# Kernel optimization log

Measured on AMD Instinct MI355X. Metric: run time of the kernel, lower is better.

Reference implementation:

```python
import jax, jax.numpy as jnp
import numpy as np

B, C, H, W = 4, 256, 160, 160
N = 512
REID = 128
NUM_LAYERS = 2
BINS = 7          # adaptive_avg_pool2d target (7,7)
EPS_BN = 1e-5
EPS_NORM = 1e-12  # torch F.normalize eps


def setup_inputs() -> dict:
    key = jax.random.key(0)
    ks = jax.random.split(key, 8)
    x = jax.random.normal(ks[0], (B, C, H, W), jnp.float32)
    # valid normalized boxes: x1,y1 in [0,0.7], w,h in [0.1,0.3]
    xy1 = jax.random.uniform(ks[1], (B, N, 2), minval=0.0, maxval=0.7)
    wh = jax.random.uniform(ks[2], (B, N, 2), minval=0.1, maxval=0.3)
    bboxes = jnp.concatenate([xy1, jnp.minimum(xy1 + wh, 1.0)], axis=-1)
    # conv stack params (kaiming-ish init), BN in eval mode with running stats
    conv_w = jax.random.normal(ks[3], (NUM_LAYERS, C, C, 3, 3), jnp.float32) * np.sqrt(2.0 / (C * 9)).astype(np.float32)
    conv_b = jnp.zeros((NUM_LAYERS, C), jnp.float32)
    bn_gamma = jnp.ones((NUM_LAYERS, C), jnp.float32)
    bn_beta = jnp.zeros((NUM_LAYERS, C), jnp.float32)
    bn_mean = jnp.zeros((NUM_LAYERS, C), jnp.float32)
    bn_var = jnp.ones((NUM_LAYERS, C), jnp.float32)
    # reid_embedding MLP: Linear(C, C//2) -> ReLU -> Dropout(eval) -> Linear(C//2, REID)
    w1 = jax.random.normal(ks[4], (C // 2, C), jnp.float32) * 0.01
    b1 = jnp.zeros((C // 2,), jnp.float32)
    w2 = jax.random.normal(ks[5], (REID, C // 2), jnp.float32) * 0.01
    b2 = jnp.zeros((REID,), jnp.float32)
    return dict(x=x, bboxes=bboxes, conv_w=conv_w, conv_b=conv_b,
                bn_gamma=bn_gamma, bn_beta=bn_beta, bn_mean=bn_mean, bn_var=bn_var,
                w1=w1, b1=b1, w2=w2, b2=b2)


def _conv_bn_relu(x, w, b, gamma, beta, mean, var):
    y = jax.lax.conv_general_dilated(
        x, w, window_strides=(1, 1), padding=((1, 1), (1, 1)),
        dimension_numbers=('NCHW', 'OIHW', 'NCHW')) + b[None, :, None, None]
    scale = (gamma / jnp.sqrt(var + EPS_BN))[None, :, None, None]
    y = (y - mean[None, :, None, None]) * scale + beta[None, :, None, None]
    return jax.nn.relu(y)


def _roi_pool(S, box):
    # S: (C, H+1, W+1) integral image of the feature map; box: (4,) = x1,y1,x2,y2 in [0,1]
    x1 = jnp.clip(jnp.floor(box[0] * W).astype(jnp.int32), 0, W)
    y1 = jnp.clip(jnp.floor(box[1] * H).astype(jnp.int32), 0, H)
    x2 = jnp.clip(jnp.floor(box[2] * W).astype(jnp.int32), 0, W)
    y2 = jnp.clip(jnp.floor(box[3] * H).astype(jnp.int32), 0, H)
    valid = (x2 > x1) & (y2 > y1)
    hl = jnp.maximum(y2 - y1, 1)
    wl = jnp.maximum(x2 - x1, 1)
    i = jnp.arange(BINS)
    # PyTorch adaptive_avg_pool2d binning: [floor(i*L/B), ceil((i+1)*L/B))
    hs = y1 + (i * hl) // BINS
    he = y1 + ((i + 1) * hl + BINS - 1) // BINS
    ws = x1 + (i * wl) // BINS
    we = x1 + ((i + 1) * wl + BINS - 1) // BINS
    # bin sums via integral image -> (C, 7, 7)
    s = (S[:, he[:, None], we[None, :]] - S[:, hs[:, None], we[None, :]]
         - S[:, he[:, None], ws[None, :]] + S[:, hs[:, None], ws[None, :]])
    area = ((he - hs)[:, None] * (we - ws)[None, :]).astype(S.dtype)
    # adaptive 7x7 avg pool, then global avg pool over the 7x7 grid
    pooled = jnp.mean(s / area, axis=(1, 2))  # (C,)
    return pooled, valid


def reference(x, bboxes, conv_w, conv_b, bn_gamma, bn_beta, bn_mean, bn_var, w1, b1, w2, b2):
    f = x
    for l in range(NUM_LAYERS):
        f = _conv_bn_relu(f, conv_w[l], conv_b[l], bn_gamma[l], bn_beta[l], bn_mean[l], bn_var[l])
    # integral image, zero-padded: S[b,c,y,x] = sum of f[b,c,:y,:x] -> (B, C, H+1, W+1)
    S = jnp.pad(jnp.cumsum(jnp.cumsum(f, axis=2), axis=3), ((0, 0), (0, 0), (1, 0), (1, 0)))
    pooled, valid = jax.vmap(jax.vmap(_roi_pool, in_axes=(None, 0)), in_axes=(0, 0))(S, bboxes)
    # reid_embedding MLP (dropout is identity in eval)
    h = jax.nn.relu(jnp.einsum('bnc,hc->bnh', pooled, w1) + b1)
    feat = jnp.einsum('bnh,rh->bnr', h, w2) + b2
    feat = jnp.where(valid[..., None], feat, jnp.zeros((), feat.dtype))
    norm = jnp.maximum(jnp.linalg.norm(feat, axis=-1, keepdims=True), EPS_NORM)
    return feat / norm
```

## Files before the change

kernel.cpp:

```cpp
#include <hip/hip_runtime.h>
#include <hip/hip_bf16.h>

typedef __attribute__((ext_vector_type(8))) short s16x8;
typedef __attribute__((ext_vector_type(4))) float f32x4;


__device__ __forceinline__ void async_ld16(const void* g, void* l) {
  __builtin_amdgcn_global_load_lds(
      (const __attribute__((address_space(1))) void*)g,
      (__attribute__((address_space(3))) void*)l, 16, 0, 0);
}

__global__ __launch_bounds__(256) void zero_borders(__hip_bfloat16* __restrict__ xpad,
                                                    __hip_bfloat16* __restrict__ f1) {
  int bi = blockIdx.x;
  int buf = bi / 2576; int rem = bi - buf * 2576;
  int b = rem / 644;   int e = rem - b * 644;
  int y, x;
  if (e < 162)      { y = 0;           x = e; }
  else if (e < 324) { y = 161;         x = e - 162; }
  else if (e < 484) { y = e - 324 + 1; x = 0; }
  else              { y = e - 484 + 1; x = 161; }
  __hip_bfloat16* p = (buf ? f1 : xpad) + (((size_t)b * 162 + y) * 162 + x) * 256 + threadIdx.x;
  *p = __float2bfloat16(0.f);
}

__global__ __launch_bounds__(256) void nchw2nhwc(const float* __restrict__ x,
                                                 __hip_bfloat16* __restrict__ xpad) {
  __shared__ float tile[32][33];
  int blk = blockIdx.x;
  int xt = blk % 5;
  int ct = (blk / 5) & 7;
  int by = blk / 40;
  int b = by / 160, y = by - (by / 160) * 160;
  int tx = threadIdx.x, ty = threadIdx.y;
  const float* src = x + (((size_t)(b * 256 + ct * 32)) * 160 + y) * 160 + xt * 32 + tx;
#pragma unroll
  for (int k = 0; k < 4; k++) tile[ty * 4 + k][tx] = src[(size_t)(ty * 4 + k) * 25600];
  __syncthreads();
  __hip_bfloat16* dst = xpad + (((size_t)(b * 162 + y + 1)) * 162 + (xt * 32 + 1)) * 256 + ct * 32 + tx;
#pragma unroll
  for (int k = 0; k < 4; k++) {
    int xx = ty * 4 + k;
    dst[(size_t)xx * 256] = __float2bfloat16(tile[tx][xx]);
  }
}

__global__ __launch_bounds__(256) void pack_w(const float* __restrict__ cw,
                                              __hip_bfloat16* __restrict__ wpk) {
  int t = blockIdx.x * 256 + threadIdx.x;
  int ci = t & 255, co = (t >> 8) & 255, rest = t >> 16;
  int tap = rest % 9, l = rest / 9;
  int dy = tap / 3, dx = tap - dy * 3;
  float v = cw[((((size_t)l * 256 + co) * 256 + ci) * 3 + dy) * 3 + dx];
  wpk[(((size_t)l * 9 + tap) * 256 + co) * 256 + ci] = __float2bfloat16(v);
}

__global__ void prep_bn(const float* __restrict__ cb, const float* __restrict__ g,
                        const float* __restrict__ bt, const float* __restrict__ mn,
                        const float* __restrict__ vr, float* __restrict__ ab) {
  int t = blockIdx.x * 256 + threadIdx.x;
  float a = g[t] / sqrtf(vr[t] + 1e-5f);
  ab[t] = a;
  ab[512 + t] = (cb[t] - mn[t]) * a + bt[t];
}

__global__ __launch_bounds__(256) void pack_mlp(const float* __restrict__ w1,
                                                const float* __restrict__ w2,
                                                float* __restrict__ w1t,
                                                float* __restrict__ w2t) {
  int t = blockIdx.x * 256 + threadIdx.x;
  if (t < 32768) {
    int h = t >> 8, k = t & 255;
    w1t[k * 128 + h] = w1[h * 256 + k];
  } else {
    int u = t - 32768;
    int r = u >> 7, k = u & 127;
    w2t[k * 128 + r] = w2[r * 128 + k];
  }
}

__global__ __launch_bounds__(256, 2) void conv_bn_relu(
    const __hip_bfloat16* __restrict__ inp, __hip_bfloat16* __restrict__ outp,
    const __hip_bfloat16* __restrict__ wpk,
    const float* __restrict__ alpha, const float* __restrict__ beff) {
  __shared__ __align__(16) short As[128 * 64];
  __shared__ __align__(16) short Bs[256 * 64];
  const int t = threadIdx.x;
  const int mtile = ((blockIdx.x & 7) * 100) + (blockIdx.x >> 3);
  const int l = t & 63;
  const int wv = t >> 6;
  const int lr = l & 15, lq = l >> 4;
  const int wm = wv >> 1, wn = wv & 1;

  const int srow = t >> 3;
  const int koff = (((t & 7) ^ (srow & 7)) << 3);
  const short* inS = (const short*)inp;
  const short* wS = (const short*)wpk;
  long abase[4];
#pragma unroll
  for (int i = 0; i < 4; i++) {
    int p = mtile * 128 + i * 32 + srow;
    int b = p / 25600; int r = p - b * 25600; int y = r / 160; int x = r - y * 160;
    abase[i] = (((long)b * 162 + y) * 162 + x) * 256 + koff;
  }
  const long bbase = ((long)srow) * 256 + koff;

  f32x4 acc[4][8];
#pragma unroll
  for (int i = 0; i < 4; i++)
#pragma unroll
    for (int j = 0; j < 8; j++) acc[i][j] = (f32x4){0.f, 0.f, 0.f, 0.f};

#pragma unroll 1
  for (int u = 0; u < 36; ++u) {
    const int tap = u >> 2, kc = u & 3;
    const int dy = tap / 3, dx = tap - dy * 3;
    const long aoff = ((long)(dy * 162 + dx)) * 256 + kc * 64;
    const long boff = (long)tap * 65536 + kc * 64;
    __syncthreads();
#pragma unroll
    for (int i = 0; i < 4; i++)
      async_ld16(inS + abase[i] + aoff, As + i * 2048 + t * 8);
#pragma unroll
    for (int j = 0; j < 8; j++)
      async_ld16(wS + bbase + boff + (long)j * 8192, Bs + j * 2048 + t * 8);
    __syncthreads();
#pragma unroll
    for (int kk = 0; kk < 2; ++kk) {
      const int ps = (((kk << 2) | lq) ^ (lr & 7)) << 3;
      s16x8 av[4], bv[8];
#pragma unroll
      for (int mi = 0; mi < 4; ++mi)
        av[mi] = *(const s16x8*)&As[(wm * 64 + mi * 16 + lr) * 64 + ps];
#pragma unroll
      for (int ni = 0; ni < 8; ++ni)
        bv[ni] = *(const s16x8*)&Bs[(wn * 128 + ni * 16 + lr) * 64 + ps];
      __builtin_amdgcn_s_setprio(1);
#pragma unroll
      for (int mi = 0; mi < 4; ++mi)
#pragma unroll
        for (int ni = 0; ni < 8; ++ni)
          acc[mi][ni] = __builtin_amdgcn_mfma_f32_16x16x32_bf16(av[mi], bv[ni], acc[mi][ni], 0, 0, 0);
      __builtin_amdgcn_s_setprio(0);
    }
  }

  float al[8], be_[8];
#pragma unroll
  for (int ni = 0; ni < 8; ++ni) {
    int co = wn * 128 + ni * 16 + lr;
    al[ni] = alpha[co];
    be_[ni] = beff[co];
  }
#pragma unroll
  for (int mi = 0; mi < 4; ++mi) {
    int prow = mtile * 128 + wm * 64 + mi * 16 + lq * 4;
#pragma unroll
    for (int j = 0; j < 4; ++j) {
      int p = prow + j;
      int b = p / 25600; int r = p - b * 25600; int y = r / 160; int x = r - y * 160;
      long ob = (((long)b * 162 + (y + 1)) * 162 + (x + 1)) * 256 + wn * 128;
#pragma unroll
      for (int ni = 0; ni < 8; ++ni) {
        float v = acc[mi][ni][j] * al[ni] + be_[ni];
        outp[ob + ni * 16 + lr] = __float2bfloat16(fmaxf(v, 0.f));
      }
    }
  }
}

__global__ __launch_bounds__(256) void cumsum_w(const __hip_bfloat16* __restrict__ f2,
                                                float* __restrict__ S) {
  int row = blockIdx.x * 2 + (threadIdx.x >> 7);
  int b = row / 160, y = row - (row / 160) * 160;
  int cp = threadIdx.x & 127;
  const unsigned* src =
      (const unsigned*)((const short*)f2 + (((size_t)b * 162 + y + 1) * 162 + 1) * 256) + cp;
  float2* dst = (float2*)(S + (((size_t)b * 161 + y + 1) * 161) * 256) + cp;
  dst[0] = float2{0.f, 0.f};
  float r0 = 0.f, r1 = 0.f;
  for (int x4 = 0; x4 < 160; x4 += 4) {
    unsigned v[4];
#pragma unroll
    for (int k = 0; k < 4; k++) v[k] = src[(size_t)(x4 + k) * 128];
#pragma unroll
    for (int k = 0; k < 4; k++) {
      r0 += __uint_as_float((v[k] & 0xffffu) << 16);
      r1 += __uint_as_float(v[k] & 0xffff0000u);
      dst[(size_t)(x4 + k + 1) * 128] = float2{r0, r1};
    }
  }
}

__global__ __launch_bounds__(256) void cumsum_h(float* __restrict__ S) {
  int bi = blockIdx.x;
  int b = bi / 161, q = bi - (bi / 161) * 161;
  int c = threadIdx.x;
  float* col = S + (((size_t)b * 161) * 161 + q) * 256 + c;
  const size_t ys = (size_t)161 * 256;
  col[0] = 0.f;
  float run = 0.f;
  for (int y0 = 1; y0 <= 160; y0 += 8) {
    float v[8];
#pragma unroll
    for (int k = 0; k < 8; k++) v[k] = col[(size_t)(y0 + k) * ys];
#pragma unroll
    for (int k = 0; k < 8; k++) { run += v[k]; col[(size_t)(y0 + k) * ys] = run; }
  }
}

__global__ __launch_bounds__(256) void roi_pool(const float* __restrict__ S,
                                                const float* __restrict__ bbox,
                                                float* __restrict__ pooled,
                                                int* __restrict__ valid) {
  int bn = blockIdx.x;
  int b = bn >> 9;
  int c = threadIdx.x;
  float bx1 = bbox[bn * 4 + 0], by1 = bbox[bn * 4 + 1];
  float bx2 = bbox[bn * 4 + 2], by2 = bbox[bn * 4 + 3];
  int x1 = min(max((int)floorf(bx1 * 160.f), 0), 160);
  int y1 = min(max((int)floorf(by1 * 160.f), 0), 160);
  int x2 = min(max((int)floorf(bx2 * 160.f), 0), 160);
  int y2 = min(max((int)floorf(by2 * 160.f), 0), 160);
  int vld = (x2 > x1 && y2 > y1) ? 1 : 0;
  int hl = max(y2 - y1, 1), wl = max(x2 - x1, 1);
  int hs[7], he[7], ws_[7], we_[7];
  float rh[7], rw[7];
#pragma unroll
  for (int i = 0; i < 7; i++) {
    hs[i] = y1 + (i * hl) / 7;
    he[i] = y1 + ((i + 1) * hl + 6) / 7;
    rh[i] = 1.f / (float)(he[i] - hs[i]);
    ws_[i] = x1 + (i * wl) / 7;
    we_[i] = x1 + ((i + 1) * wl + 6) / 7;
    rw[i] = 1.f / (float)(we_[i] - ws_[i]);
  }
  const float* Sb = S + (size_t)b * 161 * 161 * 256 + c;
  float acc = 0.f;
#pragma unroll
  for (int i = 0; i < 7; i++) {
    const float* rE = Sb + (size_t)he[i] * (161 * 256);
    const float* rS = Sb + (size_t)hs[i] * (161 * 256);
#pragma unroll
    for (int j = 0; j < 7; j++) {
      size_t qe = (size_t)we_[j] * 256, qs = (size_t)ws_[j] * 256;
      float s = rE[qe] - rS[qe] - rE[qs] + rS[qs];
      acc += s * (rh[i] * rw[j]);
    }
  }
  pooled[(size_t)bn * 256 + c] = acc * (1.f / 49.f);
  if (c == 0) valid[bn] = vld;
}

__global__ __launch_bounds__(128) void mlp_norm(const float* __restrict__ pooled,
                                                const int* __restrict__ valid,
                                                const float* __restrict__ w1t,
                                                const float* __restrict__ b1,
                                                const float* __restrict__ w2t,
                                                const float* __restrict__ b2,
                                                float* __restrict__ out) {
  int bn = blockIdx.x;
  int t = threadIdx.x;
  __shared__ float pl[256];
  __shared__ float hh[128];
  __shared__ float red[2];
  pl[t] = pooled[(size_t)bn * 256 + t];
  pl[t + 128] = pooled[(size_t)bn * 256 + 128 + t];
  __syncthreads();
  float a = b1[t];
#pragma unroll 8
  for (int k = 0; k < 256; k++) a += w1t[k * 128 + t] * pl[k];
  hh[t] = fmaxf(a, 0.f);
  __syncthreads();
  float f = b2[t];
#pragma unroll 8
  for (int k = 0; k < 128; k++) f += w2t[k * 128 + t] * hh[k];
  if (!valid[bn]) f = 0.f;
  float ss = f * f;
#pragma unroll
  for (int off = 32; off > 0; off >>= 1) ss += __shfl_xor(ss, off);
  if ((t & 63) == 0) red[t >> 6] = ss;
  __syncthreads();
  float nrm = fmaxf(sqrtf(red[0] + red[1]), 1e-12f);
  out[(size_t)bn * 128 + t] = f / nrm;
}

extern "C" void kernel_launch(void* const* d_in, const int* in_sizes, int n_in,
                              void* d_out, int out_size, void* d_ws, size_t ws_size,
                              hipStream_t stream) {
  const float* x = (const float*)d_in[0];
  const float* bboxes = (const float*)d_in[1];
  const float* conv_w = (const float*)d_in[2];
  const float* conv_b = (const float*)d_in[3];
  const float* bn_g = (const float*)d_in[4];
  const float* bn_b = (const float*)d_in[5];
  const float* bn_m = (const float*)d_in[6];
  const float* bn_v = (const float*)d_in[7];
  const float* w1 = (const float*)d_in[8];
  const float* b1 = (const float*)d_in[9];
  const float* w2 = (const float*)d_in[10];
  const float* b2 = (const float*)d_in[11];

  char* ws = (char*)d_ws;
  const size_t PADB = (size_t)4 * 162 * 162 * 256 * 2;
  const size_t WPKB = (size_t)2 * 9 * 256 * 256 * 2;
  const size_t SB = (size_t)4 * 161 * 161 * 256 * 4;
  const size_t PLB = (size_t)4 * 512 * 256 * 4;

  __hip_bfloat16* xpad = (__hip_bfloat16*)(ws);
  __hip_bfloat16* f1 = (__hip_bfloat16*)(ws + PADB);
  __hip_bfloat16* wpk = (__hip_bfloat16*)(ws + 2 * PADB);
  float* abuf = (float*)(ws + 2 * PADB + WPKB);
  float* S = (float*)(ws + 2 * PADB + WPKB + 4096);
  float* pooled = (float*)(ws + 2 * PADB + WPKB + 4096 + SB);
  int* valid = (int*)(ws + 2 * PADB + WPKB + 4096 + SB + PLB);
  float* w1t = (float*)(ws + 2 * PADB + WPKB + 4096 + SB + PLB + 8192);
  float* w2t = w1t + 32768;

  zero_borders<<<5152, 256, 0, stream>>>(xpad, f1);
  nchw2nhwc<<<25600, dim3(32, 8), 0, stream>>>(x, xpad);
  pack_w<<<4608, 256, 0, stream>>>(conv_w, wpk);
  prep_bn<<<2, 256, 0, stream>>>(conv_b, bn_g, bn_b, bn_m, bn_v, abuf);
  pack_mlp<<<192, 256, 0, stream>>>(w1, w2, w1t, w2t);

  conv_bn_relu<<<800, 256, 0, stream>>>(xpad, f1, wpk, abuf, abuf + 512);
  conv_bn_relu<<<800, 256, 0, stream>>>(f1, xpad, wpk + (size_t)9 * 256 * 256, abuf + 256, abuf + 768);

  cumsum_w<<<320, 256, 0, stream>>>(xpad, S);
  cumsum_h<<<644, 256, 0, stream>>>(S);
  roi_pool<<<2048, 256, 0, stream>>>(S, bboxes, pooled, valid);
  mlp_norm<<<2048, 128, 0, stream>>>(pooled, valid, w1t, b1, w2t, b2, (float*)d_out);
}
```

Measured before the change: 403.9 us.

## Merge prep kernels, fuse ROI pooling with MLP, retune cumsum and transpose

Merges the border zeroing, weight packing, BN prep and MLP weight transposes into one launch. Fuses roi_pool and mlp_norm so pooled features stay in shared memory instead of going through global memory. Also makes the NCHW-to-NHWC transpose handle two rows per block, gives cumsum_w one row per 128-thread block, and unrolls cumsum_h by 16. It removes the s_setprio hints around the MFMA loop in the conv kernel. The fused ROI/MLP kernel leaves half its threads idle during the MLP phase, and dropping setprio may change how waves are scheduled in the conv.

```diff
diff --git a/kernel.cpp b/kernel.cpp
--- a/kernel.cpp
+++ b/kernel.cpp
@@ -11,18 +11,48 @@
       (__attribute__((address_space(3))) void*)l, 16, 0, 0);
 }
 
-__global__ __launch_bounds__(256) void zero_borders(__hip_bfloat16* __restrict__ xpad,
-                                                    __hip_bfloat16* __restrict__ f1) {
+__global__ __launch_bounds__(256) void prep_all(
+    __hip_bfloat16* __restrict__ xpad, __hip_bfloat16* __restrict__ f1,
+    const float* __restrict__ cw, __hip_bfloat16* __restrict__ wpk,
+    const float* __restrict__ cb, const float* __restrict__ g,
+    const float* __restrict__ bt, const float* __restrict__ mn,
+    const float* __restrict__ vr, float* __restrict__ ab,
+    const float* __restrict__ w1, const float* __restrict__ w2,
+    float* __restrict__ w1t, float* __restrict__ w2t) {
   int bi = blockIdx.x;
-  int buf = bi / 2576; int rem = bi - buf * 2576;
-  int b = rem / 644;   int e = rem - b * 644;
-  int y, x;
-  if (e < 162)      { y = 0;           x = e; }
-  else if (e < 324) { y = 161;         x = e - 162; }
-  else if (e < 484) { y = e - 324 + 1; x = 0; }
-  else              { y = e - 484 + 1; x = 161; }
-  __hip_bfloat16* p = (buf ? f1 : xpad) + (((size_t)b * 162 + y) * 162 + x) * 256 + threadIdx.x;
-  *p = __float2bfloat16(0.f);
+  if (bi < 5152) {
+    int buf = bi / 2576; int rem = bi - buf * 2576;
+    int b = rem / 644;   int e = rem - b * 644;
+    int y, x;
+    if (e < 162)      { y = 0;           x = e; }
+    else if (e < 324) { y = 161;         x = e - 162; }
+    else if (e < 484) { y = e - 324 + 1; x = 0; }
+    else              { y = e - 484 + 1; x = 161; }
+    __hip_bfloat16* p = (buf ? f1 : xpad) + (((size_t)b * 162 + y) * 162 + x) * 256 + threadIdx.x;
+    *p = __float2bfloat16(0.f);
+  } else if (bi < 9760) {
+    int t = (bi - 5152) * 256 + threadIdx.x;
+    int ci = t & 255, co = (t >> 8) & 255, rest = t >> 16;
+    int tap = rest % 9, l = rest / 9;
+    int dy = tap / 3, dx = tap - dy * 3;
+    float v = cw[((((size_t)l * 256 + co) * 256 + ci) * 3 + dy) * 3 + dx];
+    wpk[(((size_t)l * 9 + tap) * 256 + co) * 256 + ci] = __float2bfloat16(v);
+  } else if (bi < 9762) {
+    int t = (bi - 9760) * 256 + threadIdx.x;
+    float a = g[t] / sqrtf(vr[t] + 1e-5f);
+    ab[t] = a;
+    ab[512 + t] = (cb[t] - mn[t]) * a + bt[t];
+  } else {
+    int t = (bi - 9762) * 256 + threadIdx.x;
+    if (t < 32768) {
+      int h = t >> 8, k = t & 255;
+      w1t[k * 128 + h] = w1[h * 256 + k];
+    } else {
+      int u = t - 32768;
+      int r = u >> 7, k = u & 127;
+      w2t[k * 128 + r] = w2[r * 128 + k];
+    }
+  }
 }
 
 __global__ __launch_bounds__(256) void nchw2nhwc(const float* __restrict__ x,
@@ -32,51 +62,22 @@
   int xt = blk % 5;
   int ct = (blk / 5) & 7;
   int by = blk / 40;
-  int b = by / 160, y = by - (by / 160) * 160;
+  int b = by / 80, yp = by - (by / 80) * 80;
   int tx = threadIdx.x, ty = threadIdx.y;
-  const float* src = x + (((size_t)(b * 256 + ct * 32)) * 160 + y) * 160 + xt * 32 + tx;
-#pragma unroll
-  for (int k = 0; k < 4; k++) tile[ty * 4 + k][tx] = src[(size_t)(ty * 4 + k) * 25600];
-  __syncthreads();
-  __hip_bfloat16* dst = xpad + (((size_t)(b * 162 + y + 1)) * 162 + (xt * 32 + 1)) * 256 + ct * 32 + tx;
-#pragma unroll
-  for (int k = 0; k < 4; k++) {
-    int xx = ty * 4 + k;
-    dst[(size_t)xx * 256] = __float2bfloat16(tile[tx][xx]);
-  }
-}
-
-__global__ __launch_bounds__(256) void pack_w(const float* __restrict__ cw,
-                                              __hip_bfloat16* __restrict__ wpk) {
-  int t = blockIdx.x * 256 + threadIdx.x;
-  int ci = t & 255, co = (t >> 8) & 255, rest = t >> 16;
-  int tap = rest % 9, l = rest / 9;
-  int dy = tap / 3, dx = tap - dy * 3;
-  float v = cw[((((size_t)l * 256 + co) * 256 + ci) * 3 + dy) * 3 + dx];
-  wpk[(((size_t)l * 9 + tap) * 256 + co) * 256 + ci] = __float2bfloat16(v);
-}
-
-__global__ void prep_bn(const float* __restrict__ cb, const float* __restrict__ g,
-                        const float* __restrict__ bt, const float* __restrict__ mn,
-                        const float* __restrict__ vr, float* __restrict__ ab) {
-  int t = blockIdx.x * 256 + threadIdx.x;
-  float a = g[t] / sqrtf(vr[t] + 1e-5f);
-  ab[t] = a;
-  ab[512 + t] = (cb[t] - mn[t]) * a + bt[t];
-}
-
-__global__ __launch_bounds__(256) void pack_mlp(const float* __restrict__ w1,
-                                                const float* __restrict__ w2,
-                                                float* __restrict__ w1t,
-                                                float* __restrict__ w2t) {
-  int t = blockIdx.x * 256 + threadIdx.x;
-  if (t < 32768) {
-    int h = t >> 8, k = t & 255;
-    w1t[k * 128 + h] = w1[h * 256 + k];
-  } else {
-    int u = t - 32768;
-    int r = u >> 7, k = u & 127;
-    w2t[k * 128 + r] = w2[r * 128 + k];
+#pragma unroll
+  for (int ry = 0; ry < 2; ++ry) {
+    int y = yp * 2 + ry;
+    const float* src = x + (((size_t)(b * 256 + ct * 32)) * 160 + y) * 160 + xt * 32 + tx;
+#pragma unroll
+    for (int k = 0; k < 4; k++) tile[ty * 4 + k][tx] = src[(size_t)(ty * 4 + k) * 25600];
+    __syncthreads();
+    __hip_bfloat16* dst = xpad + (((size_t)(b * 162 + y + 1)) * 162 + (xt * 32 + 1)) * 256 + ct * 32 + tx;
+#pragma unroll
+    for (int k = 0; k < 4; k++) {
+      int xx = ty * 4 + k;
+      dst[(size_t)xx * 256] = __float2bfloat16(tile[tx][xx]);
+    }
+    __syncthreads();
   }
 }
 
@@ -136,13 +137,11 @@
 #pragma unroll
       for (int ni = 0; ni < 8; ++ni)
         bv[ni] = *(const s16x8*)&Bs[(wn * 128 + ni * 16 + lr) * 64 + ps];
-      __builtin_amdgcn_s_setprio(1);
 #pragma unroll
       for (int mi = 0; mi < 4; ++mi)
 #pragma unroll
         for (int ni = 0; ni < 8; ++ni)
           acc[mi][ni] = __builtin_amdgcn_mfma_f32_16x16x32_bf16(av[mi], bv[ni], acc[mi][ni], 0, 0, 0);
-      __builtin_amdgcn_s_setprio(0);
     }
   }
 
@@ -170,11 +169,11 @@
   }
 }
 
-__global__ __launch_bounds__(256) void cumsum_w(const __hip_bfloat16* __restrict__ f2,
+__global__ __launch_bounds__(128) void cumsum_w(const __hip_bfloat16* __restrict__ f2,
                                                 float* __restrict__ S) {
-  int row = blockIdx.x * 2 + (threadIdx.x >> 7);
+  int row = blockIdx.x;
   int b = row / 160, y = row - (row / 160) * 160;
-  int cp = threadIdx.x & 127;
+  int cp = threadIdx.x;
   const unsigned* src =
       (const unsigned*)((const short*)f2 + (((size_t)b * 162 + y + 1) * 162 + 1) * 256) + cp;
   float2* dst = (float2*)(S + (((size_t)b * 161 + y + 1) * 161) * 256) + cp;
@@ -201,22 +200,29 @@
   const size_t ys = (size_t)161 * 256;
   col[0] = 0.f;
   float run = 0.f;
-  for (int y0 = 1; y0 <= 160; y0 += 8) {
-    float v[8];
-#pragma unroll
-    for (int k = 0; k < 8; k++) v[k] = col[(size_t)(y0 + k) * ys];
-#pragma unroll
-    for (int k = 0; k < 8; k++) { run += v[k]; col[(size_t)(y0 + k) * ys] = run; }
-  }
-}
-
-__global__ __launch_bounds__(256) void roi_pool(const float* __restrict__ S,
-                                                const float* __restrict__ bbox,
-                                                float* __restrict__ pooled,
-                                                int* __restrict__ valid) {
+  for (int y0 = 1; y0 <= 160; y0 += 16) {
+    float v[16];
+#pragma unroll
+    for (int k = 0; k < 16; k++) v[k] = col[(size_t)(y0 + k) * ys];
+#pragma unroll
+    for (int k = 0; k < 16; k++) { run += v[k]; col[(size_t)(y0 + k) * ys] = run; }
+  }
+}
+
+__global__ __launch_bounds__(256) void roi_mlp(const float* __restrict__ S,
+                                               const float* __restrict__ bbox,
+                                               const float* __restrict__ w1t,
+                                               const float* __restrict__ b1,
+                                               const float* __restrict__ w2t,
+                                               const float* __restrict__ b2,
+                                               float* __restrict__ out) {
   int bn = blockIdx.x;
   int b = bn >> 9;
-  int c = threadIdx.x;
+  int t = threadIdx.x;
+  __shared__ float pl[256];
+  __shared__ float hh[128];
+  __shared__ float red[2];
+
   float bx1 = bbox[bn * 4 + 0], by1 = bbox[bn * 4 + 1];
   float bx2 = bbox[bn * 4 + 2], by2 = bbox[bn * 4 + 3];
   int x1 = min(max((int)floorf(bx1 * 160.f), 0), 160);
@@ -236,7 +242,7 @@
     we_[i] = x1 + ((i + 1) * wl + 6) / 7;
     rw[i] = 1.f / (float)(we_[i] - ws_[i]);
   }
-  const float* Sb = S + (size_t)b * 161 * 161 * 256 + c;
+  const float* Sb = S + (size_t)b * 161 * 161 * 256 + t;
   float acc = 0.f;
 #pragma unroll
   for (int i = 0; i < 7; i++) {
@@ -249,41 +255,33 @@
       acc += s * (rh[i] * rw[j]);
     }
   }
-  pooled[(size_t)bn * 256 + c] = acc * (1.f / 49.f);
-  if (c == 0) valid[bn] = vld;
-}
-
-__global__ __launch_bounds__(128) void mlp_norm(const float* __restrict__ pooled,
-                                                const int* __restrict__ valid,
-                                                const float* __restrict__ w1t,
-                                                const float* __restrict__ b1,
-                                                const float* __restrict__ w2t,
-                                                const float* __restrict__ b2,
-                                                float* __restrict__ out) {
-  int bn = blockIdx.x;
-  int t = threadIdx.x;
-  __shared__ float pl[256];
-  __shared__ float hh[128];
-  __shared__ float red[2];
-  pl[t] = pooled[(size_t)bn * 256 + t];
-  pl[t + 128] = pooled[(size_t)bn * 256 + 128 + t];
+  pl[t] = acc * (1.f / 49.f);
   __syncthreads();
-  float a = b1[t];
+
+  float a = 0.f;
+  if (t < 128) {
+    a = b1[t];
 #pragma unroll 8
-  for (int k = 0; k < 256; k++) a += w1t[k * 128 + t] * pl[k];
-  hh[t] = fmaxf(a, 0.f);
+    for (int k = 0; k < 256; k++) a += w1t[k * 128 + t] * pl[k];
+    hh[t] = fmaxf(a, 0.f);
+  }
   __syncthreads();
-  float f = b2[t];
+  float f = 0.f;
+  if (t < 128) {
+    f = b2[t];
 #pragma unroll 8
-  for (int k = 0; k < 128; k++) f += w2t[k * 128 + t] * hh[k];
-  if (!valid[bn]) f = 0.f;
-  float ss = f * f;
-#pragma unroll
-  for (int off = 32; off > 0; off >>= 1) ss += __shfl_xor(ss, off);
-  if ((t & 63) == 0) red[t >> 6] = ss;
+    for (int k = 0; k < 128; k++) f += w2t[k * 128 + t] * hh[k];
+    if (!vld) f = 0.f;
+    float ss = f * f;
+#pragma unroll
+    for (int off = 32; off > 0; off >>= 1) ss += __shfl_xor(ss, off);
+    if ((t & 63) == 0) red[t >> 6] = ss;
+  }
   __syncthreads();
-  float nrm = fmaxf(sqrtf(red[0] + red[1]), 1e-12f);
-  out[(size_t)bn * 128 + t] = f / nrm;
+  if (t < 128) {
+    float nrm = fmaxf(sqrtf(red[0] + red[1]), 1e-12f);
+    out[(size_t)bn * 128 + t] = f / nrm;
+  }
 }
 
 extern "C" void kernel_launch(void* const* d_in, const int* in_sizes, int n_in,
@@ -306,29 +304,23 @@
   const size_t PADB = (size_t)4 * 162 * 162 * 256 * 2;
   const size_t WPKB = (size_t)2 * 9 * 256 * 256 * 2;
   const size_t SB = (size_t)4 * 161 * 161 * 256 * 4;
-  const size_t PLB = (size_t)4 * 512 * 256 * 4;
 
   __hip_bfloat16* xpad = (__hip_bfloat16*)(ws);
   __hip_bfloat16* f1 = (__hip_bfloat16*)(ws + PADB);
   __hip_bfloat16* wpk = (__hip_bfloat16*)(ws + 2 * PADB);
   float* abuf = (float*)(ws + 2 * PADB + WPKB);
   float* S = (float*)(ws + 2 * PADB + WPKB + 4096);
-  float* pooled = (float*)(ws + 2 * PADB + WPKB + 4096 + SB);
-  int* valid = (int*)(ws + 2 * PADB + WPKB + 4096 + SB + PLB);
-  float* w1t = (float*)(ws + 2 * PADB + WPKB + 4096 + SB + PLB + 8192);
+  float* w1t = (float*)(ws + 2 * PADB + WPKB + 4096 + SB);
   float* w2t = w1t + 32768;
 
-  zero_borders<<<5152, 256, 0, stream>>>(xpad, f1);
-  nchw2nhwc<<<25600, dim3(32, 8), 0, stream>>>(x, xpad);
-  pack_w<<<4608, 256, 0, stream>>>(conv_w, wpk);
-  prep_bn<<<2, 256, 0, stream>>>(conv_b, bn_g, bn_b, bn_m, bn_v, abuf);
-  pack_mlp<<<192, 256, 0, stream>>>(w1, w2, w1t, w2t);
+  prep_all<<<9954, 256, 0, stream>>>(xpad, f1, conv_w, wpk, conv_b, bn_g, bn_b, bn_m,
+                                     bn_v, abuf, w1, w2, w1t, w2t);
+  nchw2nhwc<<<12800, dim3(32, 8), 0, stream>>>(x, xpad);
 
   conv_bn_relu<<<800, 256, 0, stream>>>(xpad, f1, wpk, abuf, abuf + 512);
   conv_bn_relu<<<800, 256, 0, stream>>>(f1, xpad, wpk + (size_t)9 * 256 * 256, abuf + 256, abuf + 768);
 
-  cumsum_w<<<320, 256, 0, stream>>>(xpad, S);
+  cumsum_w<<<640, 128, 0, stream>>>(xpad, S);
   cumsum_h<<<644, 256, 0, stream>>>(S);
-  roi_pool<<<2048, 256, 0, stream>>>(S, bboxes, pooled, valid);
-  mlp_norm<<<2048, 128, 0, stream>>>(pooled, valid, w1t, b1, w2t, b2, (float*)d_out);
-}
+  roi_mlp<<<2048, 256, 0, stream>>>(S, bboxes, w1t, b1, w2t, b2, (float*)d_out);
+}
```

After: 407.5 us. Within noise of the previous version (+0.9%).
